# Optimization experiments

Measured on AMD Instinct MI355X. Metric: run time of the kernel, lower is better.

Reference implementation:

```python
import jax, jax.numpy as jnp
import numpy as np

ALPHA = 0.5  # leakage
T, B, I, H = 512, 64, 128, 1024
SCALE = 0.9  # input_scaling
RHO = 0.99   # target spectral radius (approximated by 1/sqrt(H) normal scaling)


def setup_inputs() -> dict:
    key = jax.random.key(0)
    k1, k2, k3, k4, k5 = jax.random.split(key, 5)
    x = jax.random.normal(k1, (T, B, I), dtype=jnp.float32)
    # uniform(-scale, scale) kernel init
    W_in0 = jax.random.uniform(k2, (H, I), jnp.float32, -SCALE, SCALE)
    # normal recurrent init scaled so spectral radius ~= rho (circular law: radius ~ sigma*sqrt(H))
    W_hat0 = jax.random.normal(k3, (H, H), jnp.float32) * (RHO / np.sqrt(H))
    W_in1 = jax.random.uniform(k4, (H, H), jnp.float32, -SCALE, SCALE)
    W_hat1 = jax.random.normal(k5, (H, H), jnp.float32) * (RHO / np.sqrt(H))
    return {"x": x, "W_in0": W_in0, "W_hat0": W_hat0, "W_in1": W_in1, "W_hat1": W_hat1}


def _run_layer(inp, W_in, W_hat):
    # inp: [T, B, F_in]; returns full state trajectory [T, B, H]
    def step(h, x_t):
        pre = x_t @ W_in.T + h @ W_hat.T          # [B, H]
        h_new = (1.0 - ALPHA) * h + ALPHA * jnp.tanh(pre)
        return h_new, h_new

    h0 = jnp.zeros((inp.shape[1], W_hat.shape[0]), dtype=inp.dtype)
    _, ys = jax.lax.scan(step, h0, inp)
    return ys


def reference(x, W_in0, W_hat0, W_in1, W_hat1):
    e0 = _run_layer(x, W_in0, W_hat0)   # layer 0 states [T, B, H]
    e1 = _run_layer(e0, W_in1, W_hat1)  # layer 1 states [T, B, H]
    return jnp.stack([e0, e1], axis=-2)  # [T, B, num_layers, H]
```

## Files before the change

kernel.cpp:

```cpp
#include <hip/hip_runtime.h>
#include <math.h>

#define TSTEPS 512
#define BATCH  64
#define HDIM   1024
#define IDIM   128
#define NBLOCKS 256
#define NTHR   512
#define NCNT   64

typedef __attribute__((ext_vector_type(8))) short bf16x8;
typedef __attribute__((ext_vector_type(4))) float f32x4;
typedef __attribute__((ext_vector_type(4))) unsigned u32x4;

#define WI0HI 0
#define WI0LO (WI0HI + 1024*128)
#define WH0HI (WI0LO + 1024*128)
#define WH0LO (WH0HI + 1024*1024)
#define WI1HI (WH0LO + 1024*1024)
#define WI1LO (WI1HI + 1024*1024)
#define WH1HI (WI1LO + 1024*1024)
#define WH1LO (WH1HI + 1024*1024)
#define WS_USHORTS (WH1LO + 1024*1024)
#define CNT_OFF_BYTES ((size_t)WS_USHORTS * 2)

#define L0_WI_HI 0
#define L0_WI_LO (L0_WI_HI + 16*136*2)
#define L0_WH_HI (L0_WI_LO + 16*136*2)
#define L0_WH_LO (L0_WH_HI + 16*1032*2)
#define L1_WI_HI 0
#define L1_WI_LO (L1_WI_HI + 16*1032*2)
#define L1_WH_HI (L1_WI_LO + 16*1032*2)
#define L1_WH_LO (L1_WH_HI + 16*1032*2)
#define WLDS_BYTES (L1_WH_LO + 16*1032*2)

__device__ __forceinline__ unsigned short bf_hi(float f) {
    unsigned u = __builtin_bit_cast(unsigned, f);
    unsigned r = u + 0x7fffu + ((u >> 16) & 1u);
    return (unsigned short)(r >> 16);
}
__device__ __forceinline__ float bf_tof(unsigned short h) {
    unsigned u = ((unsigned)h) << 16;
    return __builtin_bit_cast(float, u);
}

__device__ __forceinline__ void split8(const float* __restrict__ p,
                                       bf16x8& ah, bf16x8& al) {
    f32x4 a = *(const f32x4*)p, b = *(const f32x4*)(p + 4);
    float fv[8] = {a[0], a[1], a[2], a[3], b[0], b[1], b[2], b[3]};
    u32x4 H, L;
    #pragma unroll
    for (int q = 0; q < 4; ++q) {
        const float f0 = fv[2 * q], f1 = fv[2 * q + 1];
        unsigned h;
        asm("v_cvt_pk_bf16_f32 %0, %1, %2" : "=v"(h) : "v"(f0), "v"(f1));
        const float h0 = __builtin_bit_cast(float, h << 16);
        const float h1 = __builtin_bit_cast(float, h & 0xffff0000u);
        unsigned lo;
        asm("v_cvt_pk_bf16_f32 %0, %1, %2" : "=v"(lo) : "v"(f0 - h0), "v"(f1 - h1));
        H[q] = h; L[q] = lo;
    }
    ah = __builtin_bit_cast(bf16x8, H);
    al = __builtin_bit_cast(bf16x8, L);
}

__device__ __forceinline__ void ks_step(const float* __restrict__ asrc,
    const unsigned char* __restrict__ lds, int hiOff, int loOff,
    int stride, int kcol, int lr, f32x4& acc)
{
    bf16x8 ah, al;
    split8(asrc, ah, al);
    const int bo = (lr * stride + kcol) * 2;
    bf16x8 bh = *(const bf16x8*)(&lds[hiOff + bo]);
    bf16x8 bl = *(const bf16x8*)(&lds[loOff + bo]);
    acc = __builtin_amdgcn_mfma_f32_16x16x32_bf16(ah, bh, acc, 0, 0, 0);
    acc = __builtin_amdgcn_mfma_f32_16x16x32_bf16(al, bh, acc, 0, 0, 0);
    acc = __builtin_amdgcn_mfma_f32_16x16x32_bf16(ah, bl, acc, 0, 0, 0);
}

template<int K>
__device__ __forceinline__ void stage_w(const unsigned short* __restrict__ g,
        unsigned char* __restrict__ lds, int ldsOff, int jbase, int tid)
{
    constexpr int TOT = 16 * K;
    #pragma unroll
    for (int base = 0; base < TOT; base += NTHR * 8) {
        const int e = base + tid * 8;
        if (TOT >= NTHR * 8 || e < TOT) {
            const int j = e / K, k = e % K;
            uint4 v = *(const uint4*)(g + (size_t)(jbase + j) * K + k);
            *(uint4*)(&lds[ldsOff + (j * (K + 8) + k) * 2]) = v;
        }
    }
}

__global__ void prep_kernel(const float* __restrict__ Wi0, const float* __restrict__ Wh0,
                            const float* __restrict__ Wi1, const float* __restrict__ Wh1,
                            unsigned short* __restrict__ wsU)
{
    const int n = 1024*128 + 3*1024*1024;
    for (int e = blockIdx.x * blockDim.x + threadIdx.x; e < n;
         e += gridDim.x * blockDim.x) {
        const float* src; int idx, hiOff, loOff;
        if (e < 1024*128)            { src = Wi0; idx = e;              hiOff = WI0HI; loOff = WI0LO; }
        else if (e < 1024*128 + 1024*1024)   { src = Wh0; idx = e - 1024*128;   hiOff = WH0HI; loOff = WH0LO; }
        else if (e < 1024*128 + 2*1024*1024) { src = Wi1; idx = e - 1024*128 - 1024*1024; hiOff = WI1HI; loOff = WI1LO; }
        else                         { src = Wh1; idx = e - 1024*128 - 2*1024*1024; hiOff = WH1HI; loOff = WH1LO; }
        float f = src[idx];
        unsigned short h = bf_hi(f);
        wsU[hiOff + idx] = h;
        wsU[loOff + idx] = bf_hi(f - bf_tof(h));
    }
}

__device__ __forceinline__ void grid_barrier(unsigned* cntBase, unsigned epoch) {
    __syncthreads();
    const int tid = (int)threadIdx.x;
    if (tid == 0)
        __hip_atomic_fetch_add(cntBase + (blockIdx.x & (NCNT - 1)) * 16, 1u,
                               __ATOMIC_RELAXED, __HIP_MEMORY_SCOPE_AGENT);
    if (tid < 64) {
        const unsigned tgt = (NBLOCKS / NCNT) * epoch;
        for (;;) {
            unsigned v = __hip_atomic_load(cntBase + tid * 16, __ATOMIC_RELAXED,
                                           __HIP_MEMORY_SCOPE_AGENT);
            if (__ballot(v >= tgt) == ~0ull) break;
            __builtin_amdgcn_s_sleep(1);
        }
    }
    __syncthreads();
}

__global__ __launch_bounds__(NTHR) void reservoir_kernel(
    const float* __restrict__ x, float* __restrict__ out,
    const unsigned short* __restrict__ wsU, unsigned* __restrict__ cnt)
{
    __shared__ __align__(16) unsigned char wlds[WLDS_BYTES];
    __shared__ f32x4 red[8 * 64];

    const int bid = blockIdx.x;
    const int layer = bid >> 7;
    const int rr  = bid & 127;
    const int jt  = rr >> 1, mh = rr & 1;
    const int tid = (int)threadIdx.x;
    const int w   = __builtin_amdgcn_readfirstlane(tid >> 6);
    const int m2  = w & 1, kh = w >> 1;
    const int l   = tid & 63, lr = l & 15, tq = l >> 4;
    const int jbase = jt * 16;
    const int rowb  = mh * 32 + m2 * 16;

    if (layer == 0) {
        stage_w<128 >(wsU + WI0HI, wlds, L0_WI_HI, jbase, tid);
        stage_w<128 >(wsU + WI0LO, wlds, L0_WI_LO, jbase, tid);
        stage_w<1024>(wsU + WH0HI, wlds, L0_WH_HI, jbase, tid);
        stage_w<1024>(wsU + WH0LO, wlds, L0_WH_LO, jbase, tid);
    } else {
        stage_w<1024>(wsU + WI1HI, wlds, L1_WI_HI, jbase, tid);
        stage_w<1024>(wsU + WI1LO, wlds, L1_WI_LO, jbase, tid);
        stage_w<1024>(wsU + WH1HI, wlds, L1_WH_HI, jbase, tid);
        stage_w<1024>(wsU + WH1LO, wlds, L1_WH_LO, jbase, tid);
    }
    __syncthreads();

    float hold[4] = {0.f, 0.f, 0.f, 0.f};
    const int arow = rowb + lr;

    for (int i = 0; i <= TSTEPS; ++i) {
        const int t = layer ? (i - 1) : i;
        const bool valid = layer ? (t >= 0) : (t < TSTEPS);
        if (valid) {
            f32x4 accA = {0.f, 0.f, 0.f, 0.f};
            f32x4 accB = {0.f, 0.f, 0.f, 0.f};
            if (layer == 0) {
                {
                    const int kb = kh * 32 + tq * 8;
                    ks_step(x + (size_t)t * (BATCH * IDIM) + arow * IDIM + kb,
                            wlds, L0_WI_HI, L0_WI_LO, 136, kb, lr, accA);
                }
                if (t >= 1) {
                    const float* h0 = out + (size_t)(t - 1) * 131072 + arow * 2048;
                    #pragma unroll 4
                    for (int ks = 0; ks < 8; ++ks) {
                        const int kb = kh * 256 + ks * 32 + tq * 8;
                        ks_step(h0 + kb, wlds, L0_WH_HI, L0_WH_LO, 1032, kb, lr,
                                (ks & 1) ? accA : accB);
                    }
                }
            } else {
                if (kh < 2) {
                    const float* e0 = out + (size_t)t * 131072 + arow * 2048;
                    #pragma unroll 4
                    for (int ks = 0; ks < 16; ++ks) {
                        const int kb = kh * 512 + ks * 32 + tq * 8;
                        ks_step(e0 + kb, wlds, L1_WI_HI, L1_WI_LO, 1032, kb, lr,
                                (ks & 1) ? accA : accB);
                    }
                } else if (t >= 1) {
                    const float* h1 = out + (size_t)(t - 1) * 131072 + arow * 2048 + 1024;
                    #pragma unroll 4
                    for (int ks = 0; ks < 16; ++ks) {
                        const int kb = (kh - 2) * 512 + ks * 32 + tq * 8;
                        ks_step(h1 + kb, wlds, L1_WH_HI, L1_WH_LO, 1032, kb, lr,
                                (ks & 1) ? accA : accB);
                    }
                }
            }

            red[w * 64 + l] = accA + accB;
            __syncthreads();
            if (w < 2) {
                f32x4 s  = red[(w + 0) * 64 + l];
                f32x4 s1 = red[(w + 2) * 64 + l];
                f32x4 s2 = red[(w + 4) * 64 + l];
                f32x4 s3 = red[(w + 6) * 64 + l];
                #pragma unroll
                for (int r = 0; r < 4; ++r) {
                    const float pre = ((s[r] + s1[r]) + (s2[r] + s3[r]));
                    const float hnew = 0.5f * hold[r] + 0.5f * tanhf(pre);
                    hold[r] = hnew;
                    const int row = mh * 32 + w * 16 + tq * 4 + r;
                    const int col = jbase + lr;
                    float* dst = out + (size_t)t * 131072 + row * 2048 + layer * 1024 + col;
                    __hip_atomic_store(dst, hnew, __ATOMIC_RELAXED, __HIP_MEMORY_SCOPE_AGENT);
                }
            }
            __syncthreads();
        }
        if (i < TSTEPS)
            grid_barrier(cnt, (unsigned)(i + 1));
    }
}

extern "C" void kernel_launch(void* const* d_in, const int* in_sizes, int n_in,
                              void* d_out, int out_size, void* d_ws, size_t ws_size,
                              hipStream_t stream) {
    const float* x   = (const float*)d_in[0];
    const float* Wi0 = (const float*)d_in[1];
    const float* Wh0 = (const float*)d_in[2];
    const float* Wi1 = (const float*)d_in[3];
    const float* Wh1 = (const float*)d_in[4];
    float* out = (float*)d_out;
    unsigned short* wsU = (unsigned short*)d_ws;
    unsigned* cnt = (unsigned*)((char*)d_ws + CNT_OFF_BYTES);

    hipMemsetAsync((char*)d_ws + CNT_OFF_BYTES, 0, NCNT * 64, stream);
    prep_kernel<<<256, 256, 0, stream>>>(Wi0, Wh0, Wi1, Wh1, wsU);

    void* args[] = {(void*)&x, (void*)&out, (void*)&wsU, (void*)&cnt};
    hipLaunchCooperativeKernel((const void*)reservoir_kernel,
                               dim3(NBLOCKS), dim3(NTHR), args, 0, stream);
}
```

Before: 4.895 ms.

## Keep weight fragments in registers and use a centralized grid barrier

Each lane now loads its bf16 hi/lo weight fragments once into registers (32 bf16x8 vectors) instead of staging them in LDS and re-reading them every step. This removes per-step LDS traffic and the large shared allocation. The grid barrier now has block 0 poll the 64 counters and publish a release flag, and every other block spins on that single flag instead of scanning all counters. launch_bounds is raised to 2 blocks per CU. The costs are heavier register pressure and an extra hop through the flag in each barrier.

```diff
diff --git a/kernel.cpp b/kernel.cpp
--- a/kernel.cpp
+++ b/kernel.cpp
@@ -23,16 +23,6 @@
 #define WH1LO (WH1HI + 1024*1024)
 #define WS_USHORTS (WH1LO + 1024*1024)
 #define CNT_OFF_BYTES ((size_t)WS_USHORTS * 2)
-
-#define L0_WI_HI 0
-#define L0_WI_LO (L0_WI_HI + 16*136*2)
-#define L0_WH_HI (L0_WI_LO + 16*136*2)
-#define L0_WH_LO (L0_WH_HI + 16*1032*2)
-#define L1_WI_HI 0
-#define L1_WI_LO (L1_WI_HI + 16*1032*2)
-#define L1_WH_HI (L1_WI_LO + 16*1032*2)
-#define L1_WH_LO (L1_WH_HI + 16*1032*2)
-#define WLDS_BYTES (L1_WH_LO + 16*1032*2)
 
 __device__ __forceinline__ unsigned short bf_hi(float f) {
     unsigned u = __builtin_bit_cast(unsigned, f);
@@ -64,34 +54,13 @@
     al = __builtin_bit_cast(bf16x8, L);
 }
 
-__device__ __forceinline__ void ks_step(const float* __restrict__ asrc,
-    const unsigned char* __restrict__ lds, int hiOff, int loOff,
-    int stride, int kcol, int lr, f32x4& acc)
-{
+__device__ __forceinline__ void ks_r(const float* __restrict__ asrc,
+                                     bf16x8 bh, bf16x8 bl, f32x4& acc) {
     bf16x8 ah, al;
     split8(asrc, ah, al);
-    const int bo = (lr * stride + kcol) * 2;
-    bf16x8 bh = *(const bf16x8*)(&lds[hiOff + bo]);
-    bf16x8 bl = *(const bf16x8*)(&lds[loOff + bo]);
     acc = __builtin_amdgcn_mfma_f32_16x16x32_bf16(ah, bh, acc, 0, 0, 0);
     acc = __builtin_amdgcn_mfma_f32_16x16x32_bf16(al, bh, acc, 0, 0, 0);
     acc = __builtin_amdgcn_mfma_f32_16x16x32_bf16(ah, bl, acc, 0, 0, 0);
-}
-
-template<int K>
-__device__ __forceinline__ void stage_w(const unsigned short* __restrict__ g,
-        unsigned char* __restrict__ lds, int ldsOff, int jbase, int tid)
-{
-    constexpr int TOT = 16 * K;
-    #pragma unroll
-    for (int base = 0; base < TOT; base += NTHR * 8) {
-        const int e = base + tid * 8;
-        if (TOT >= NTHR * 8 || e < TOT) {
-            const int j = e / K, k = e % K;
-            uint4 v = *(const uint4*)(g + (size_t)(jbase + j) * K + k);
-            *(uint4*)(&lds[ldsOff + (j * (K + 8) + k) * 2]) = v;
-        }
-    }
 }
 
 __global__ void prep_kernel(const float* __restrict__ Wi0, const float* __restrict__ Wh0,
@@ -119,23 +88,31 @@
     if (tid == 0)
         __hip_atomic_fetch_add(cntBase + (blockIdx.x & (NCNT - 1)) * 16, 1u,
                                __ATOMIC_RELAXED, __HIP_MEMORY_SCOPE_AGENT);
-    if (tid < 64) {
-        const unsigned tgt = (NBLOCKS / NCNT) * epoch;
-        for (;;) {
-            unsigned v = __hip_atomic_load(cntBase + tid * 16, __ATOMIC_RELAXED,
-                                           __HIP_MEMORY_SCOPE_AGENT);
-            if (__ballot(v >= tgt) == ~0ull) break;
+    if (blockIdx.x == 0) {
+        if (tid < 64) {
+            const unsigned tgt = (NBLOCKS / NCNT) * epoch;
+            for (;;) {
+                unsigned v = __hip_atomic_load(cntBase + tid * 16, __ATOMIC_RELAXED,
+                                               __HIP_MEMORY_SCOPE_AGENT);
+                if (__ballot(v >= tgt) == ~0ull) break;
+                __builtin_amdgcn_s_sleep(1);
+            }
+            if (tid == 0)
+                __hip_atomic_store(cntBase + NCNT * 16, epoch,
+                                   __ATOMIC_RELAXED, __HIP_MEMORY_SCOPE_AGENT);
+        }
+    } else if (tid == 0) {
+        while (__hip_atomic_load(cntBase + NCNT * 16, __ATOMIC_RELAXED,
+                                 __HIP_MEMORY_SCOPE_AGENT) < epoch)
             __builtin_amdgcn_s_sleep(1);
-        }
     }
     __syncthreads();
 }
 
-__global__ __launch_bounds__(NTHR) void reservoir_kernel(
+__global__ __launch_bounds__(NTHR, 2) void reservoir_kernel(
     const float* __restrict__ x, float* __restrict__ out,
     const unsigned short* __restrict__ wsU, unsigned* __restrict__ cnt)
 {
-    __shared__ __align__(16) unsigned char wlds[WLDS_BYTES];
     __shared__ f32x4 red[8 * 64];
 
     const int bid = blockIdx.x;
@@ -147,23 +124,31 @@
     const int m2  = w & 1, kh = w >> 1;
     const int l   = tid & 63, lr = l & 15, tq = l >> 4;
     const int jbase = jt * 16;
-    const int rowb  = mh * 32 + m2 * 16;
-
+    const int arow  = mh * 32 + m2 * 16 + lr;
+
+    bf16x8 wfh[16], wfl[16];
     if (layer == 0) {
-        stage_w<128 >(wsU + WI0HI, wlds, L0_WI_HI, jbase, tid);
-        stage_w<128 >(wsU + WI0LO, wlds, L0_WI_LO, jbase, tid);
-        stage_w<1024>(wsU + WH0HI, wlds, L0_WH_HI, jbase, tid);
-        stage_w<1024>(wsU + WH0LO, wlds, L0_WH_LO, jbase, tid);
+        const size_t rx = (size_t)(jbase + lr) * IDIM + kh * 32 + tq * 8;
+        wfh[0] = *(const bf16x8*)(wsU + WI0HI + rx);
+        wfl[0] = *(const bf16x8*)(wsU + WI0LO + rx);
+        const size_t rh = (size_t)(jbase + lr) * HDIM + kh * 256 + tq * 8;
+        #pragma unroll
+        for (int ks = 0; ks < 8; ++ks) {
+            wfh[1 + ks] = *(const bf16x8*)(wsU + WH0HI + rh + ks * 32);
+            wfl[1 + ks] = *(const bf16x8*)(wsU + WH0LO + rh + ks * 32);
+        }
     } else {
-        stage_w<1024>(wsU + WI1HI, wlds, L1_WI_HI, jbase, tid);
-        stage_w<1024>(wsU + WI1LO, wlds, L1_WI_LO, jbase, tid);
-        stage_w<1024>(wsU + WH1HI, wlds, L1_WH_HI, jbase, tid);
-        stage_w<1024>(wsU + WH1LO, wlds, L1_WH_LO, jbase, tid);
-    }
-    __syncthreads();
+        const int hiOff = (kh < 2) ? WI1HI : WH1HI;
+        const int loOff = (kh < 2) ? WI1LO : WH1LO;
+        const size_t ro = (size_t)(jbase + lr) * HDIM + (kh & 1) * 512 + tq * 8;
+        #pragma unroll
+        for (int ks = 0; ks < 16; ++ks) {
+            wfh[ks] = *(const bf16x8*)(wsU + hiOff + ro + ks * 32);
+            wfl[ks] = *(const bf16x8*)(wsU + loOff + ro + ks * 32);
+        }
+    }
 
     float hold[4] = {0.f, 0.f, 0.f, 0.f};
-    const int arow = rowb + lr;
 
     for (int i = 0; i <= TSTEPS; ++i) {
         const int t = layer ? (i - 1) : i;
@@ -172,37 +157,26 @@
             f32x4 accA = {0.f, 0.f, 0.f, 0.f};
             f32x4 accB = {0.f, 0.f, 0.f, 0.f};
             if (layer == 0) {
-                {
-                    const int kb = kh * 32 + tq * 8;
-                    ks_step(x + (size_t)t * (BATCH * IDIM) + arow * IDIM + kb,
-                            wlds, L0_WI_HI, L0_WI_LO, 136, kb, lr, accA);
-                }
+                ks_r(x + (size_t)t * (BATCH * IDIM) + arow * IDIM + kh * 32 + tq * 8,
+                     wfh[0], wfl[0], accA);
                 if (t >= 1) {
-                    const float* h0 = out + (size_t)(t - 1) * 131072 + arow * 2048;
-                    #pragma unroll 4
-                    for (int ks = 0; ks < 8; ++ks) {
-                        const int kb = kh * 256 + ks * 32 + tq * 8;
-                        ks_step(h0 + kb, wlds, L0_WH_HI, L0_WH_LO, 1032, kb, lr,
-                                (ks & 1) ? accA : accB);
-                    }
+                    const float* h0 = out + (size_t)(t - 1) * 131072 + arow * 2048
+                                      + kh * 256 + tq * 8;
+                    #pragma unroll
+                    for (int ks = 0; ks < 8; ++ks)
+                        ks_r(h0 + ks * 32, wfh[1 + ks], wfl[1 + ks],
+                             (ks & 1) ? accA : accB);
                 }
             } else {
-                if (kh < 2) {
-                    const float* e0 = out + (size_t)t * 131072 + arow * 2048;
-                    #pragma unroll 4
-                    for (int ks = 0; ks < 16; ++ks) {
-                        const int kb = kh * 512 + ks * 32 + tq * 8;
-                        ks_step(e0 + kb, wlds, L1_WI_HI, L1_WI_LO, 1032, kb, lr,
-                                (ks & 1) ? accA : accB);
-                    }
-                } else if (t >= 1) {
-                    const float* h1 = out + (size_t)(t - 1) * 131072 + arow * 2048 + 1024;
-                    #pragma unroll 4
-                    for (int ks = 0; ks < 16; ++ks) {
-                        const int kb = (kh - 2) * 512 + ks * 32 + tq * 8;
-                        ks_step(h1 + kb, wlds, L1_WH_HI, L1_WH_LO, 1032, kb, lr,
-                                (ks & 1) ? accA : accB);
-                    }
+                const bool doit = (kh < 2) || (t >= 1);
+                if (doit) {
+                    const int ts  = (kh < 2) ? t : (t - 1);
+                    const float* src = out + (size_t)ts * 131072 + arow * 2048
+                                       + ((kh < 2) ? 0 : 1024) + (kh & 1) * 512 + tq * 8;
+                    #pragma unroll
+                    for (int ks = 0; ks < 16; ++ks)
+                        ks_r(src + ks * 32, wfh[ks], wfl[ks],
+                             (ks & 1) ? accA : accB);
                 }
             }
 
@@ -243,7 +217,7 @@
     unsigned short* wsU = (unsigned short*)d_ws;
     unsigned* cnt = (unsigned*)((char*)d_ws + CNT_OFF_BYTES);
 
-    hipMemsetAsync((char*)d_ws + CNT_OFF_BYTES, 0, NCNT * 64, stream);
+    hipMemsetAsync((char*)d_ws + CNT_OFF_BYTES, 0, NCNT * 64 + 64, stream);
     prep_kernel<<<256, 256, 0, stream>>>(Wi0, Wh0, Wi1, Wh1, wsU);
 
     void* args[] = {(void*)&x, (void*)&out, (void*)&wsU, (void*)&cnt};
```

Result: no change. 4.846 ms (-1.0%).
